# Kernel optimization log

Measured on AMD Instinct MI355X. Metric: run time of the kernel, lower is better.

## Reference

```python
import jax, jax.numpy as jnp
import numpy as np

B, T, D, H, NW = 2, 2048, 1024, 16, 64
HD = D // H  # 64
EPS = 1e-12  # F.normalize eps


def setup_inputs() -> dict:
    key = jax.random.key(0)
    ks = jax.random.split(key, 8)
    def lin(k, din, dout):
        return jax.random.normal(k, (din, dout), jnp.float32) / np.sqrt(din).astype(np.float32)
    return {
        "x": jax.random.normal(ks[0], (B, T, D), jnp.float32),
        "Wqf": lin(ks[1], D, H * NW), "bqf": jnp.zeros((H * NW,), jnp.float32),
        "Wkf": lin(ks[2], D, H * NW), "bkf": jnp.zeros((H * NW,), jnp.float32),
        "Wqp": lin(ks[3], D, H * NW), "bqp": jnp.zeros((H * NW,), jnp.float32),
        "Wkp": lin(ks[4], D, H * NW), "bkp": jnp.zeros((H * NW,), jnp.float32),
        "Wv": lin(ks[5], D, D), "bv": jnp.zeros((D,), jnp.float32),
        "Wo": lin(ks[6], D, D), "bo": jnp.zeros((D,), jnp.float32),
        "scale": jnp.ones((H, 1, 1), jnp.float32),  # interference_scale
    }


def reference(x, Wqf, bqf, Wkf, bkf, Wqp, bqp, Wkp, bkp, Wv, bv, Wo, bo, scale):
    Bx, Tx, Dx = x.shape
    def heads(W, b, nd):  # [B,T,H*nd] -> [B,H,T,nd]
        return jnp.transpose((x @ W + b).reshape(Bx, Tx, H, nd), (0, 2, 1, 3))
    qf = heads(Wqf, bqf, NW); kf = heads(Wkf, bkf, NW)
    qp = heads(Wqp, bqp, NW); kp = heads(Wkp, bkp, NW)
    v = heads(Wv, bv, HD)
    t = jnp.arange(Tx, dtype=x.dtype)[None, None, :, None]  # [1,1,T,1]
    def wave_norm(f, p):
        w = jnp.sin(f * t + p)  # [B,H,T,NW]
        n = jnp.sqrt(jnp.sum(w * w, axis=-1, keepdims=True))
        return w / jnp.maximum(n, EPS)
    qn = wave_norm(qf, qp)
    kn = wave_norm(kf, kp)
    inter = jnp.einsum('bhtw,bhsw->bhts', qn, kn) * scale[None]  # [B,H,T,T]
    causal = jnp.tril(jnp.ones((Tx, Tx), bool))  # keep diag and below
    inter = jnp.where(causal, inter, jnp.zeros((), x.dtype))
    denom = jnp.sqrt(jnp.arange(1, Tx + 1, dtype=x.dtype))[:, None]  # [T,1]
    attn = inter / denom
    # dropout is identity in eval mode
    out = jnp.einsum('bhts,bhsd->bhtd', attn, v)
    out = jnp.transpose(out, (0, 2, 1, 3)).reshape(Bx, Tx, Dx)
    return out @ Wo + bo
```

## Files before the change

kernel.cpp:

```cpp
#include <hip/hip_runtime.h>


#define Bb 2
#define Tt 2048
#define Dd 1024
#define Hh 16
#define NC 32

typedef _Float16 half_t;
typedef _Float16 half8 __attribute__((ext_vector_type(8)));
typedef _Float16 half4h __attribute__((ext_vector_type(4)));
typedef float f32x16 __attribute__((ext_vector_type(16)));

#define MFMA32(a, b, c) __builtin_amdgcn_mfma_f32_32x32x16_f16((a), (b), (c), 0, 0, 0)

#define GLL(G, L) __builtin_amdgcn_global_load_lds(                      \
    (const __attribute__((address_space(1))) void*)(G),                  \
    (__attribute__((address_space(3))) void*)(L), 16, 0, 0)

#define SCHED_FENCE() __builtin_amdgcn_sched_barrier(0)

#define BARC() {                                                         \
    asm volatile("s_waitcnt vmcnt(4) lgkmcnt(0)" ::: "memory");          \
    __builtin_amdgcn_s_barrier(); }

#define BAR_LG() {                                                       \
    SCHED_FENCE();                                                       \
    asm volatile("s_waitcnt lgkmcnt(0)" ::: "memory");                   \
    __builtin_amdgcn_s_barrier();                                        \
    SCHED_FENCE(); }

__global__ __launch_bounds__(256) void xsplit_kernel(
    const float* __restrict__ X, half_t* __restrict__ XHI, half_t* __restrict__ XLO)
{
  const size_t i = ((size_t)blockIdx.x * 256 + threadIdx.x) * 8;
  float4 a = *(const float4*)&X[i];
  float4 b = *(const float4*)&X[i + 4];
  const float av[8] = {a.x, a.y, a.z, a.w, b.x, b.y, b.z, b.w};
  half8 hv, lv;
  #pragma unroll
  for (int j = 0; j < 8; ++j) {
    half_t hx = (half_t)av[j];
    hv[j] = hx; lv[j] = (half_t)((av[j] - (float)hx) * 2048.f);
  }
  *(half8*)&XHI[i] = hv;
  *(half8*)&XLO[i] = lv;
}

__global__ __launch_bounds__(256) void wsplit_kernel(
    const float* __restrict__ W0, const float* __restrict__ W1,
    const float* __restrict__ W2, const float* __restrict__ W3,
    const float* __restrict__ W4, const float* __restrict__ W5,
    half_t* __restrict__ WSP)
{
  __shared__ float Ld[64][68];
  const int tid = threadIdx.x;
  const int m = blockIdx.z;
  const float* W = (m == 0) ? W0 : (m == 1) ? W1 : (m == 2) ? W2
                 : (m == 3) ? W3 : (m == 4) ? W4 : W5;
  const int k0 = blockIdx.x * 64, n0 = blockIdx.y * 64;
  const int r = tid >> 2, c4 = (tid & 3) * 16;
  #pragma unroll
  for (int i = 0; i < 4; ++i)
    *(float4*)&Ld[r][c4 + i * 4] =
        *(const float4*)&W[(size_t)(k0 + r) * Dd + n0 + c4 + i * 4];
  __syncthreads();
  half_t* hi = WSP + (size_t)m * 2097152;
  half_t* lo = hi + 1048576;
  const int n = tid >> 2, kc = (tid & 3) * 16;
  half8 hv0, hv1, lv0, lv1;
  #pragma unroll
  for (int i = 0; i < 8; ++i) {
    float v0 = Ld[kc + i][n];
    half_t h0 = (half_t)v0;
    hv0[i] = h0; lv0[i] = (half_t)((v0 - (float)h0) * 2048.f);
    float v1 = Ld[kc + 8 + i][n];
    half_t h1 = (half_t)v1;
    hv1[i] = h1; lv1[i] = (half_t)((v1 - (float)h1) * 2048.f);
  }
  *(half8*)&hi[(size_t)(n0 + n) * Dd + k0 + kc]     = hv0;
  *(half8*)&hi[(size_t)(n0 + n) * Dd + k0 + kc + 8] = hv1;
  *(half8*)&lo[(size_t)(n0 + n) * Dd + k0 + kc]     = lv0;
  *(half8*)&lo[(size_t)(n0 + n) * Dd + k0 + kc + 8] = lv1;
}

__global__ __launch_bounds__(256, 2) void proj_kernel(
    const half_t* __restrict__ XHI, const half_t* __restrict__ XLO,
    const half_t* __restrict__ WSP,
    const float* __restrict__ bqf, const float* __restrict__ bqp,
    const float* __restrict__ bkf, const float* __restrict__ bkp,
    half_t* __restrict__ QNH, half_t* __restrict__ KNH)
{
  __shared__ __align__(16) half_t Bs[4][128][64];
  const int tid = threadIdx.x;
  const int mb = blockIdx.x, h = blockIdx.y;
  const int b = blockIdx.z >> 1, p = blockIdx.z & 1;
  const int t0 = mb * 128, row0 = b * Tt + t0, col0 = h * 64;
  const half_t* WF = WSP + (size_t)(2 * p) * 2097152;
  const half_t* WP = WSP + (size_t)(2 * p + 1) * 2097152;
  const float* BF = p ? bkf : bqf;
  const float* BP = p ? bkp : bqp;
  half_t* OUTH = p ? KNH : QNH;

  f32x16 hh[4], mx[4];
  #pragma unroll
  for (int i = 0; i < 4; ++i) { hh[i] = (f32x16)(0.f); mx[i] = (f32x16)(0.f); }

  const int lane = tid & 63, w = tid >> 6;
  const int rl = lane & 31, kq = lane >> 5;
  const int sw = rl & 7;

  const half_t* aHi = XHI + (size_t)(row0 + 32 * w + rl) * Dd + kq * 8;
  const half_t* aLo = XLO + (size_t)(row0 + 32 * w + rl) * Dd + kq * 8;

  const int lr8 = lane >> 3;
  const int lcc = (lane & 7) ^ lr8;
  const int csel = (lcc & 3) * 8;
  const size_t loOff = (lcc >= 4) ? 1048576 : 0;
  const half_t* gb0 = WF + loOff + (size_t)(col0 + 8 * w + lr8) * Dd + csel;
  const half_t* gb1 = gb0 + 32 * Dd;
  const half_t* gb2 = WP + loOff + (size_t)(col0 + 8 * w + lr8) * Dd + csel;
  const half_t* gb3 = gb2 + 32 * Dd;

#define STAGE_PB(BI, K) {                          \
    GLL(gb0 + (K), &Bs[BI][8 * w][0]);             \
    GLL(gb1 + (K), &Bs[BI][32 + 8 * w][0]);        \
    GLL(gb2 + (K), &Bs[BI][64 + 8 * w][0]);        \
    GLL(gb3 + (K), &Bs[BI][96 + 8 * w][0]); }

#define LOADA(H0, H1, L0, L1, K) {                 \
    H0 = *(const half8*)&aHi[(K)];                 \
    H1 = *(const half8*)&aHi[(K) + 16];            \
    L0 = *(const half8*)&aLo[(K)];                 \
    L1 = *(const half8*)&aLo[(K) + 16]; }

#define KT_P(H0, H1, L0, L1, BI) {                                     \
    { const int c0 = (kq ^ sw) * 8, c1 = ((4 + kq) ^ sw) * 8;          \
      _Pragma("unroll")                                                \
      for (int tn = 0; tn < 4; ++tn) {                                 \
        half8 bh = *(const half8*)&Bs[BI][32 * tn + rl][c0];           \
        half8 bl = *(const half8*)&Bs[BI][32 * tn + rl][c1];           \
        hh[tn] = MFMA32(H0, bh, hh[tn]);                               \
        mx[tn] = MFMA32(H0, bl, mx[tn]);                               \
        mx[tn] = MFMA32(L0, bh, mx[tn]); } }                           \
    { const int c0 = (((2 + kq)) ^ sw) * 8, c1 = ((6 + kq) ^ sw) * 8;  \
      _Pragma("unroll")                                                \
      for (int tn = 0; tn < 4; ++tn) {                                 \
        half8 bh = *(const half8*)&Bs[BI][32 * tn + rl][c0];           \
        half8 bl = *(const half8*)&Bs[BI][32 * tn + rl][c1];           \
        hh[tn] = MFMA32(H1, bh, hh[tn]);                               \
        mx[tn] = MFMA32(H1, bl, mx[tn]);                               \
        mx[tn] = MFMA32(L1, bh, mx[tn]); } } }

  half8 ah0c, ah1c, al0c, al1c, ah0n, ah1n, al0n, al1n;
  STAGE_PB(0, 0)
  STAGE_PB(1, 32)
  LOADA(ah0c, ah1c, al0c, al1c, 0)
  BARC()

  #pragma unroll 1
  for (int k0 = 0; k0 < Dd; k0 += 128) {
    LOADA(ah0n, ah1n, al0n, al1n, k0 + 32)
    STAGE_PB(2, k0 + 64)
    KT_P(ah0c, ah1c, al0c, al1c, 0)
    BARC()
    LOADA(ah0c, ah1c, al0c, al1c, k0 + 64)
    STAGE_PB(3, k0 + 96)
    KT_P(ah0n, ah1n, al0n, al1n, 1)
    BARC()
    LOADA(ah0n, ah1n, al0n, al1n, k0 + 96)
    if (k0 + 128 < Dd) { STAGE_PB(0, k0 + 128) }
    KT_P(ah0c, ah1c, al0c, al1c, 2)
    BARC()
    if (k0 + 128 < Dd) { LOADA(ah0c, ah1c, al0c, al1c, k0 + 128) }
    if (k0 + 160 < Dd) { STAGE_PB(1, k0 + 160) }
    KT_P(ah0n, ah1n, al0n, al1n, 3)
    BARC()
  }
#undef STAGE_PB
#undef LOADA
#undef KT_P

  const float bf0 = BF[col0 + rl], bf1 = BF[col0 + 32 + rl];
  const float bp0 = BP[col0 + rl], bp1 = BP[col0 + 32 + rl];
  #pragma unroll
  for (int j = 0; j < 16; ++j) {
    const int rtj = (j & 3) + 8 * (j >> 2) + 4 * kq;
    const float tf = (float)(t0 + 32 * w + rtj);
    float f0 = hh[0][j] + mx[0][j] * (1.f / 2048.f) + bf0;
    float f1 = hh[1][j] + mx[1][j] * (1.f / 2048.f) + bf1;
    float p0 = hh[2][j] + mx[2][j] * (1.f / 2048.f) + bp0;
    float p1 = hh[3][j] + mx[3][j] * (1.f / 2048.f) + bp1;
    float w0 = sinf(fmaf(f0, tf, p0));
    float w1 = sinf(fmaf(f1, tf, p1));
    float ss = w0 * w0 + w1 * w1;
    ss += __shfl_xor(ss, 1); ss += __shfl_xor(ss, 2);
    ss += __shfl_xor(ss, 4); ss += __shfl_xor(ss, 8);
    ss += __shfl_xor(ss, 16);
    const float inv = 1.f / fmaxf(sqrtf(ss), 1e-12f);
    half_t* op = &OUTH[((size_t)(b * Tt) + t0 + 32 * w + rtj) * Dd + col0];
    op[rl]      = (half_t)(w0 * inv);
    op[32 + rl] = (half_t)(w1 * inv);
  }
}

__global__ __launch_bounds__(256, 2) void gemm_kernel(
    const half_t* __restrict__ AHI, const half_t* __restrict__ ALO,
    const half_t* __restrict__ WHI,
    const float* __restrict__ BIAS, float* __restrict__ OUT)
{
  __shared__ __align__(16) half_t As[2][128][64];
  __shared__ __align__(16) half_t Bs[2][128][64];
  const int tid = threadIdx.x;
  const int m0 = blockIdx.x * 128, n0 = blockIdx.y * 128;

  f32x16 hh[4], mx[4];
  #pragma unroll
  for (int i = 0; i < 4; ++i) { hh[i] = (f32x16)(0.f); mx[i] = (f32x16)(0.f); }

  const int lane = tid & 63, w = tid >> 6;
  const int rl = lane & 31, kq = lane >> 5;
  const int sw = rl & 7;

  const int r = tid & 127, isB = tid >> 7;
  const int swr = r & 7;
  const half_t* srcHi = isB ? &WHI[(size_t)(n0 + r) * Dd]
                            : &AHI[(size_t)(m0 + r) * Dd];
  const half_t* srcLo = isB ? &WHI[1048576 + (size_t)(n0 + r) * Dd]
                            : &ALO[(size_t)(m0 + r) * Dd];
  half_t* dstRow = isB ? &Bs[0][r][0] : &As[0][r][0];
  const int pc0 = (0 ^ swr) * 8, pc1 = (1 ^ swr) * 8;
  const int pc2 = (2 ^ swr) * 8, pc3 = (3 ^ swr) * 8;
  const int pc4 = (4 ^ swr) * 8, pc5 = (5 ^ swr) * 8;
  const int pc6 = (6 ^ swr) * 8, pc7 = (7 ^ swr) * 8;

  half8 rg0, rg1, rg2, rg3, rg4, rg5, rg6, rg7;

#define G_LOADREGS(K)                                                          \
  rg0 = *(const half8*)&srcHi[(K)];      rg1 = *(const half8*)&srcHi[(K) + 8]; \
  rg2 = *(const half8*)&srcHi[(K) + 16]; rg3 = *(const half8*)&srcHi[(K) + 24];\
  rg4 = *(const half8*)&srcLo[(K)];      rg5 = *(const half8*)&srcLo[(K) + 8]; \
  rg6 = *(const half8*)&srcLo[(K) + 16]; rg7 = *(const half8*)&srcLo[(K) + 24];

#define G_WRITE(BI) {                                                     \
  half_t* d_ = dstRow + (BI) * 8192;                                      \
  *(half8*)&d_[pc0] = rg0; *(half8*)&d_[pc1] = rg1;                       \
  *(half8*)&d_[pc2] = rg2; *(half8*)&d_[pc3] = rg3;                       \
  *(half8*)&d_[pc4] = rg4; *(half8*)&d_[pc5] = rg5;                       \
  *(half8*)&d_[pc6] = rg6; *(half8*)&d_[pc7] = rg7; }

#define G_KT(BI)                                                          \
  _Pragma("unroll")                                                       \
  for (int ks = 0; ks < 2; ++ks) {                                        \
    half8 ahi = *(const half8*)&As[BI][32 * w + rl][((2 * ks + kq) ^ sw) * 8];       \
    half8 alo = *(const half8*)&As[BI][32 * w + rl][((4 + 2 * ks + kq) ^ sw) * 8];   \
    _Pragma("unroll")                                                     \
    for (int tn = 0; tn < 4; ++tn) {                                      \
      half8 bhi = *(const half8*)&Bs[BI][32 * tn + rl][((2 * ks + kq) ^ sw) * 8];    \
      half8 blo = *(const half8*)&Bs[BI][32 * tn + rl][((4 + 2 * ks + kq) ^ sw) * 8];\
      hh[tn] = MFMA32(ahi, bhi, hh[tn]);                                  \
      mx[tn] = MFMA32(ahi, blo, mx[tn]);                                  \
      mx[tn] = MFMA32(alo, bhi, mx[tn]);                                  \
    }                                                                     \
  }

  G_LOADREGS(0)
  G_WRITE(0)
  G_LOADREGS(32)
  BAR_LG()

  #pragma unroll 1
  for (int k0 = 0; k0 < Dd; k0 += 64) {
    G_KT(0)
    G_WRITE(1)
    if (k0 + 64 < Dd) { G_LOADREGS(k0 + 64) }
    BAR_LG()
    G_KT(1)
    if (k0 + 64 < Dd) { G_WRITE(0) }
    if (k0 + 96 < Dd) { G_LOADREGS(k0 + 96) }
    BAR_LG()
  }
#undef G_LOADREGS
#undef G_WRITE
#undef G_KT

  const float bb0 = BIAS[n0 + rl],      bb1 = BIAS[n0 + 32 + rl];
  const float bb2 = BIAS[n0 + 64 + rl], bb3 = BIAS[n0 + 96 + rl];
  #pragma unroll
  for (int j = 0; j < 16; ++j) {
    const int rtj = (j & 3) + 8 * (j >> 2) + 4 * kq;
    float* orow = &OUT[(size_t)(m0 + 32 * w + rtj) * Dd + n0];
    orow[rl]      = hh[0][j] + mx[0][j] * (1.f / 2048.f) + bb0;
    orow[32 + rl] = hh[1][j] + mx[1][j] * (1.f / 2048.f) + bb1;
    orow[64 + rl] = hh[2][j] + mx[2][j] * (1.f / 2048.f) + bb2;
    orow[96 + rl] = hh[3][j] + mx[3][j] * (1.f / 2048.f) + bb3;
  }
}

__global__ __launch_bounds__(256) void chunk_kv_kernel(
    const half_t* __restrict__ KNH, const float* __restrict__ V,
    float* __restrict__ G)
{
  __shared__ float Ks[64][64];
  __shared__ float Vs[64][64];
  const int tid = threadIdx.x;
  const int c = blockIdx.x, h = blockIdx.y, b = blockIdx.z;
  const int s0 = c * 64;
  const int lr = tid >> 2, lc = (tid & 3) * 16;
  {
    const half_t* krow = &KNH[(size_t)(b * Tt + s0 + lr) * Dd + h * 64 + lc];
    half8 ka = *(const half8*)&krow[0];
    half8 kb = *(const half8*)&krow[8];
    #pragma unroll
    for (int i = 0; i < 8; ++i) {
      Ks[lr][lc + i] = (float)ka[i];
      Ks[lr][lc + 8 + i] = (float)kb[i];
    }
    const float* vrow = &V[(size_t)(b * Tt + s0 + lr) * Dd + h * 64 + lc];
    #pragma unroll
    for (int i = 0; i < 4; ++i)
      *(float4*)&Vs[lr][lc + i * 4] = *(const float4*)&vrow[i * 4];
  }
  __syncthreads();

  const int ty = tid >> 4, tx = tid & 15;
  float g[4][4] = {{0.f}};
  #pragma unroll 4
  for (int s = 0; s < 64; ++s) {
    float4 kv = *(const float4*)&Ks[s][ty * 4];
    float4 vv = *(const float4*)&Vs[s][tx * 4];
    const float* k_ = (const float*)&kv;
    const float* v_ = (const float*)&vv;
    #pragma unroll
    for (int i = 0; i < 4; ++i)
      #pragma unroll
      for (int j = 0; j < 4; ++j)
        g[i][j] = fmaf(k_[i], v_[j], g[i][j]);
  }
  float* Gp = G + (((size_t)(b * Hh + h) * NC + c) << 12);
  #pragma unroll
  for (int i = 0; i < 4; ++i)
    *(float4*)&Gp[(ty * 4 + i) * 64 + tx * 4] =
        make_float4(g[i][0], g[i][1], g[i][2], g[i][3]);
}

__global__ __launch_bounds__(256) void prefix_kernel(float* __restrict__ G)
{
  const int seg = blockIdx.x, h = blockIdx.y, b = blockIdx.z;
  float* base = G + (((size_t)(b * Hh + h) * NC) << 12) + seg * 256 + threadIdx.x;
  float acc = 0.f;
  #pragma unroll 4
  for (int c = 0; c < NC; ++c) {
    float* p = base + ((size_t)c << 12);
    const float g = *p;
    *p = acc;
    acc += g;
  }
}

__global__ __launch_bounds__(256) void attn_chunk_kernel(
    const half_t* __restrict__ QNH, const half_t* __restrict__ KNH,
    const float* __restrict__ V, const float* __restrict__ M,
    const float* __restrict__ SCALE,
    half_t* __restrict__ ATTHI, half_t* __restrict__ ATTLO)
{
  __shared__ float Qt[64][68];
  __shared__ float Kt[64][68];
  __shared__ float SM[64][68];
  __shared__ float Vs[64][64];
  const int tid = threadIdx.x;
  const int c = blockIdx.x, h = blockIdx.y, b = blockIdx.z;
  const int t0 = c * 64;
  const int lr = tid >> 2, lc = (tid & 3) * 16;
  {
    const half_t* qrow = &QNH[(size_t)(b * Tt + t0 + lr) * Dd + h * 64 + lc];
    const half_t* krow = &KNH[(size_t)(b * Tt + t0 + lr) * Dd + h * 64 + lc];
    half8 qa = *(const half8*)&qrow[0];
    half8 qb = *(const half8*)&qrow[8];
    half8 ka = *(const half8*)&krow[0];
    half8 kb = *(const half8*)&krow[8];
    #pragma unroll
    for (int i = 0; i < 8; ++i) {
      Qt[lc + i][lr] = (float)qa[i];     Qt[lc + 8 + i][lr] = (float)qb[i];
      Kt[lc + i][lr] = (float)ka[i];     Kt[lc + 8 + i][lr] = (float)kb[i];
    }
    const float* vrow = &V[(size_t)(b * Tt + t0 + lr) * Dd + h * 64 + lc];
    const float* mrow = &M[(((size_t)(b * Hh + h) * NC + c) << 12) + lr * 64 + lc];
    #pragma unroll
    for (int i = 0; i < 4; ++i) {
      *(float4*)&Vs[lr][lc + i * 4] = *(const float4*)&vrow[i * 4];
      *(float4*)&SM[lr][lc + i * 4] = *(const float4*)&mrow[i * 4];
    }
  }
  __syncthreads();

  const int ty = tid >> 4, tx = tid & 15;
  float o[4][4] = {{0.f}};
  float sc[4][4] = {{0.f}};

  #pragma unroll 4
  for (int w = 0; w < 64; ++w) {
    float4 qv = *(const float4*)&Qt[w][ty * 4];
    float4 mv = *(const float4*)&SM[w][tx * 4];
    float4 kv = *(const float4*)&Kt[w][tx * 4];
    const float* q_ = (const float*)&qv;
    const float* m_ = (const float*)&mv;
    const float* k_ = (const float*)&kv;
    #pragma unroll
    for (int i = 0; i < 4; ++i) {
      float qq = q_[i];
      #pragma unroll
      for (int j = 0; j < 4; ++j) {
        o[i][j]  = fmaf(qq, m_[j], o[i][j]);
        sc[i][j] = fmaf(qq, k_[j], sc[i][j]);
      }
    }
  }
  __syncthreads();

  #pragma unroll
  for (int i = 0; i < 4; ++i) {
    const int lt = ty * 4 + i;
    #pragma unroll
    for (int j = 0; j < 4; ++j) {
      const int ls = tx * 4 + j;
      SM[ls][lt] = (ls <= lt) ? sc[i][j] : 0.f;
    }
  }
  __syncthreads();

  #pragma unroll 4
  for (int s = 0; s < 64; ++s) {
    float4 sv = *(const float4*)&SM[s][ty * 4];
    float4 vv = *(const float4*)&Vs[s][tx * 4];
    const float* s_ = (const float*)&sv;
    const float* v_ = (const float*)&vv;
    #pragma unroll
    for (int i = 0; i < 4; ++i)
      #pragma unroll
      for (int j = 0; j < 4; ++j)
        o[i][j] = fmaf(s_[i], v_[j], o[i][j]);
  }

  const float sch = SCALE[h];
  #pragma unroll
  for (int i = 0; i < 4; ++i) {
    const int t = t0 + ty * 4 + i;
    const float fac = sch / sqrtf((float)(t + 1));
    half4h hv, lv;
    #pragma unroll
    for (int j = 0; j < 4; ++j) {
      float v = o[i][j] * fac;
      half_t hx = (half_t)v;
      hv[j] = hx; lv[j] = (half_t)((v - (float)hx) * 2048.f);
    }
    *(half4h*)&ATTHI[(size_t)(b * Tt + t) * Dd + h * 64 + tx * 4] = hv;
    *(half4h*)&ATTLO[(size_t)(b * Tt + t) * Dd + h * 64 + tx * 4] = lv;
  }
}

extern "C" void kernel_launch(void* const* d_in, const int* in_sizes, int n_in,
                              void* d_out, int out_size, void* d_ws, size_t ws_size,
                              hipStream_t stream) {
  const float* x   = (const float*)d_in[0];
  const float* Wqf = (const float*)d_in[1];
  const float* bqf = (const float*)d_in[2];
  const float* Wkf = (const float*)d_in[3];
  const float* bkf = (const float*)d_in[4];
  const float* Wqp = (const float*)d_in[5];
  const float* bqp = (const float*)d_in[6];
  const float* Wkp = (const float*)d_in[7];
  const float* bkp = (const float*)d_in[8];
  const float* Wv  = (const float*)d_in[9];
  const float* bv  = (const float*)d_in[10];
  const float* Wo  = (const float*)d_in[11];
  const float* bo  = (const float*)d_in[12];
  const float* scale = (const float*)d_in[13];

  half_t* WSP = (half_t*)d_ws;
  half_t* qnh = WSP + 12582912;
  half_t* knh = qnh + 4194304;
  float*  G   = (float*)(knh + 4194304);
  half_t* xhi = (half_t*)G;
  half_t* xlo = xhi + 4194304;
  float*  vbuf = (float*)d_out;

  xsplit_kernel<<<dim3(2048), 256, 0, stream>>>(x, xhi, xlo);

  wsplit_kernel<<<dim3(16, 16, 6), 256, 0, stream>>>(Wqf, Wqp, Wkf, Wkp, Wv, Wo, WSP);

  proj_kernel<<<dim3(Tt / 128, Hh, Bb * 2), 256, 0, stream>>>(
      xhi, xlo, WSP, bqf, bqp, bkf, bkp, qnh, knh);

  gemm_kernel<<<dim3((Bb * Tt) / 128, Dd / 128), 256, 0, stream>>>(
      xhi, xlo, WSP + (size_t)4 * 2097152, bv, vbuf);

  chunk_kv_kernel<<<dim3(NC, Hh, Bb), 256, 0, stream>>>(knh, vbuf, G);
  prefix_kernel<<<dim3(16, Hh, Bb), 256, 0, stream>>>(G);
  attn_chunk_kernel<<<dim3(NC, Hh, Bb), 256, 0, stream>>>(
      qnh, knh, vbuf, G, scale, qnh , knh );

  gemm_kernel<<<dim3((Bb * Tt) / 128, Dd / 128), 256, 0, stream>>>(
      qnh, knh, WSP + (size_t)5 * 2097152, bo, (float*)d_out);
}
```

Baseline: 360.5 us.

## Double proj kernel M-tile to 256 rows per block to reuse staged weights

Each wave in the projection kernel now computes two 32-row sub-tiles (64 rows) instead of one, so a block covers 256 time steps and each staged weight tile in shared memory feeds twice as many MFMAs. The grid along T is halved and launch bounds drop to one block per SM to make room for the doubled accumulators. This cuts weight re-fetch from global memory and LDS traffic per FLOP. In exchange it raises register pressure, halves the block count to 512, and loses the latency hiding that two resident blocks provided.

```diff
diff --git a/kernel.cpp b/kernel.cpp
--- a/kernel.cpp
+++ b/kernel.cpp
@@ -84,7 +84,7 @@
   *(half8*)&lo[(size_t)(n0 + n) * Dd + k0 + kc + 8] = lv1;
 }
 
-__global__ __launch_bounds__(256, 2) void proj_kernel(
+__global__ __launch_bounds__(256, 1) void proj_kernel(
     const half_t* __restrict__ XHI, const half_t* __restrict__ XLO,
     const half_t* __restrict__ WSP,
     const float* __restrict__ bqf, const float* __restrict__ bqp,
@@ -95,23 +95,28 @@
   const int tid = threadIdx.x;
   const int mb = blockIdx.x, h = blockIdx.y;
   const int b = blockIdx.z >> 1, p = blockIdx.z & 1;
-  const int t0 = mb * 128, row0 = b * Tt + t0, col0 = h * 64;
+  const int t0 = mb * 256, row0 = b * Tt + t0, col0 = h * 64;
   const half_t* WF = WSP + (size_t)(2 * p) * 2097152;
   const half_t* WP = WSP + (size_t)(2 * p + 1) * 2097152;
   const float* BF = p ? bkf : bqf;
   const float* BP = p ? bkp : bqp;
   half_t* OUTH = p ? KNH : QNH;
 
-  f32x16 hh[4], mx[4];
-  #pragma unroll
-  for (int i = 0; i < 4; ++i) { hh[i] = (f32x16)(0.f); mx[i] = (f32x16)(0.f); }
+  f32x16 hh0[4], mx0[4], hh1[4], mx1[4];
+  #pragma unroll
+  for (int i = 0; i < 4; ++i) {
+    hh0[i] = (f32x16)(0.f); mx0[i] = (f32x16)(0.f);
+    hh1[i] = (f32x16)(0.f); mx1[i] = (f32x16)(0.f);
+  }
 
   const int lane = tid & 63, w = tid >> 6;
   const int rl = lane & 31, kq = lane >> 5;
   const int sw = rl & 7;
 
-  const half_t* aHi = XHI + (size_t)(row0 + 32 * w + rl) * Dd + kq * 8;
-  const half_t* aLo = XLO + (size_t)(row0 + 32 * w + rl) * Dd + kq * 8;
+  const half_t* aHi0 = XHI + (size_t)(row0 + 64 * w + rl) * Dd + kq * 8;
+  const half_t* aLo0 = XLO + (size_t)(row0 + 64 * w + rl) * Dd + kq * 8;
+  const half_t* aHi1 = aHi0 + 32 * Dd;
+  const half_t* aLo1 = aLo0 + 32 * Dd;
 
   const int lr8 = lane >> 3;
   const int lcc = (lane & 7) ^ lr8;
@@ -128,79 +133,94 @@
     GLL(gb2 + (K), &Bs[BI][64 + 8 * w][0]);        \
     GLL(gb3 + (K), &Bs[BI][96 + 8 * w][0]); }
 
-#define LOADA(H0, H1, L0, L1, K) {                 \
-    H0 = *(const half8*)&aHi[(K)];                 \
-    H1 = *(const half8*)&aHi[(K) + 16];            \
-    L0 = *(const half8*)&aLo[(K)];                 \
-    L1 = *(const half8*)&aLo[(K) + 16]; }
-
-#define KT_P(H0, H1, L0, L1, BI) {                                     \
+#define LOADA8(R00, R01, R02, R03, R10, R11, R12, R13, K) {  \
+    R00 = *(const half8*)&aHi0[(K)];                         \
+    R01 = *(const half8*)&aHi0[(K) + 16];                    \
+    R02 = *(const half8*)&aLo0[(K)];                         \
+    R03 = *(const half8*)&aLo0[(K) + 16];                    \
+    R10 = *(const half8*)&aHi1[(K)];                         \
+    R11 = *(const half8*)&aHi1[(K) + 16];                    \
+    R12 = *(const half8*)&aLo1[(K)];                         \
+    R13 = *(const half8*)&aLo1[(K) + 16]; }
+
+#define KT2(R00, R01, R02, R03, R10, R11, R12, R13, BI) {              \
     { const int c0 = (kq ^ sw) * 8, c1 = ((4 + kq) ^ sw) * 8;          \
       _Pragma("unroll")                                                \
       for (int tn = 0; tn < 4; ++tn) {                                 \
         half8 bh = *(const half8*)&Bs[BI][32 * tn + rl][c0];           \
         half8 bl = *(const half8*)&Bs[BI][32 * tn + rl][c1];           \
-        hh[tn] = MFMA32(H0, bh, hh[tn]);                               \
-        mx[tn] = MFMA32(H0, bl, mx[tn]);                               \
-        mx[tn] = MFMA32(L0, bh, mx[tn]); } }                           \
-    { const int c0 = (((2 + kq)) ^ sw) * 8, c1 = ((6 + kq) ^ sw) * 8;  \
+        hh0[tn] = MFMA32(R00, bh, hh0[tn]);                            \
+        mx0[tn] = MFMA32(R00, bl, mx0[tn]);                            \
+        mx0[tn] = MFMA32(R02, bh, mx0[tn]);                            \
+        hh1[tn] = MFMA32(R10, bh, hh1[tn]);                            \
+        mx1[tn] = MFMA32(R10, bl, mx1[tn]);                            \
+        mx1[tn] = MFMA32(R12, bh, mx1[tn]); } }                        \
+    { const int c0 = ((2 + kq) ^ sw) * 8, c1 = ((6 + kq) ^ sw) * 8;    \
       _Pragma("unroll")                                                \
       for (int tn = 0; tn < 4; ++tn) {                                 \
         half8 bh = *(const half8*)&Bs[BI][32 * tn + rl][c0];           \
         half8 bl = *(const half8*)&Bs[BI][32 * tn + rl][c1];           \
-        hh[tn] = MFMA32(H1, bh, hh[tn]);                               \
-        mx[tn] = MFMA32(H1, bl, mx[tn]);                               \
-        mx[tn] = MFMA32(L1, bh, mx[tn]); } } }
-
-  half8 ah0c, ah1c, al0c, al1c, ah0n, ah1n, al0n, al1n;
+        hh0[tn] = MFMA32(R01, bh, hh0[tn]);                            \
+        mx0[tn] = MFMA32(R01, bl, mx0[tn]);                            \
+        mx0[tn] = MFMA32(R03, bh, mx0[tn]);                            \
+        hh1[tn] = MFMA32(R11, bh, hh1[tn]);                            \
+        mx1[tn] = MFMA32(R11, bl, mx1[tn]);                            \
+        mx1[tn] = MFMA32(R13, bh, mx1[tn]); } } }
+
+  half8 c00, c01, c02, c03, c10, c11, c12, c13;
+  half8 n00, n01, n02, n03, n10, n11, n12, n13;
   STAGE_PB(0, 0)
   STAGE_PB(1, 32)
-  LOADA(ah0c, ah1c, al0c, al1c, 0)
+  LOADA8(c00, c01, c02, c03, c10, c11, c12, c13, 0)
   BARC()
 
   #pragma unroll 1
   for (int k0 = 0; k0 < Dd; k0 += 128) {
-    LOADA(ah0n, ah1n, al0n, al1n, k0 + 32)
+    LOADA8(n00, n01, n02, n03, n10, n11, n12, n13, k0 + 32)
     STAGE_PB(2, k0 + 64)
-    KT_P(ah0c, ah1c, al0c, al1c, 0)
+    KT2(c00, c01, c02, c03, c10, c11, c12, c13, 0)
     BARC()
-    LOADA(ah0c, ah1c, al0c, al1c, k0 + 64)
+    LOADA8(c00, c01, c02, c03, c10, c11, c12, c13, k0 + 64)
     STAGE_PB(3, k0 + 96)
-    KT_P(ah0n, ah1n, al0n, al1n, 1)
+    KT2(n00, n01, n02, n03, n10, n11, n12, n13, 1)
     BARC()
-    LOADA(ah0n, ah1n, al0n, al1n, k0 + 96)
+    LOADA8(n00, n01, n02, n03, n10, n11, n12, n13, k0 + 96)
     if (k0 + 128 < Dd) { STAGE_PB(0, k0 + 128) }
-    KT_P(ah0c, ah1c, al0c, al1c, 2)
+    KT2(c00, c01, c02, c03, c10, c11, c12, c13, 2)
     BARC()
-    if (k0 + 128 < Dd) { LOADA(ah0c, ah1c, al0c, al1c, k0 + 128) }
+    if (k0 + 128 < Dd) { LOADA8(c00, c01, c02, c03, c10, c11, c12, c13, k0 + 128) }
     if (k0 + 160 < Dd) { STAGE_PB(1, k0 + 160) }
-    KT_P(ah0n, ah1n, al0n, al1n, 3)
+    KT2(n00, n01, n02, n03, n10, n11, n12, n13, 3)
     BARC()
   }
 #undef STAGE_PB
-#undef LOADA
-#undef KT_P
+#undef LOADA8
+#undef KT2
 
   const float bf0 = BF[col0 + rl], bf1 = BF[col0 + 32 + rl];
   const float bp0 = BP[col0 + rl], bp1 = BP[col0 + 32 + rl];
   #pragma unroll
-  for (int j = 0; j < 16; ++j) {
-    const int rtj = (j & 3) + 8 * (j >> 2) + 4 * kq;
-    const float tf = (float)(t0 + 32 * w + rtj);
-    float f0 = hh[0][j] + mx[0][j] * (1.f / 2048.f) + bf0;
-    float f1 = hh[1][j] + mx[1][j] * (1.f / 2048.f) + bf1;
-    float p0 = hh[2][j] + mx[2][j] * (1.f / 2048.f) + bp0;
-    float p1 = hh[3][j] + mx[3][j] * (1.f / 2048.f) + bp1;
-    float w0 = sinf(fmaf(f0, tf, p0));
-    float w1 = sinf(fmaf(f1, tf, p1));
-    float ss = w0 * w0 + w1 * w1;
-    ss += __shfl_xor(ss, 1); ss += __shfl_xor(ss, 2);
-    ss += __shfl_xor(ss, 4); ss += __shfl_xor(ss, 8);
-    ss += __shfl_xor(ss, 16);
-    const float inv = 1.f / fmaxf(sqrtf(ss), 1e-12f);
-    half_t* op = &OUTH[((size_t)(b * Tt) + t0 + 32 * w + rtj) * Dd + col0];
-    op[rl]      = (half_t)(w0 * inv);
-    op[32 + rl] = (half_t)(w1 * inv);
+  for (int g = 0; g < 2; ++g) {
+    #pragma unroll
+    for (int j = 0; j < 16; ++j) {
+      const int rtj = (j & 3) + 8 * (j >> 2) + 4 * kq;
+      const int trow = t0 + 64 * w + 32 * g + rtj;
+      const float tf = (float)trow;
+      float f0 = (g ? hh1[0][j] : hh0[0][j]) + (g ? mx1[0][j] : mx0[0][j]) * (1.f / 2048.f) + bf0;
+      float f1 = (g ? hh1[1][j] : hh0[1][j]) + (g ? mx1[1][j] : mx0[1][j]) * (1.f / 2048.f) + bf1;
+      float p0 = (g ? hh1[2][j] : hh0[2][j]) + (g ? mx1[2][j] : mx0[2][j]) * (1.f / 2048.f) + bp0;
+      float p1 = (g ? hh1[3][j] : hh0[3][j]) + (g ? mx1[3][j] : mx0[3][j]) * (1.f / 2048.f) + bp1;
+      float w0 = sinf(fmaf(f0, tf, p0));
+      float w1 = sinf(fmaf(f1, tf, p1));
+      float ss = w0 * w0 + w1 * w1;
+      ss += __shfl_xor(ss, 1); ss += __shfl_xor(ss, 2);
+      ss += __shfl_xor(ss, 4); ss += __shfl_xor(ss, 8);
+      ss += __shfl_xor(ss, 16);
+      const float inv = 1.f / fmaxf(sqrtf(ss), 1e-12f);
+      half_t* op = &OUTH[((size_t)(b * Tt) + trow) * Dd + col0];
+      op[rl]      = (half_t)(w0 * inv);
+      op[32 + rl] = (half_t)(w1 * inv);
+    }
   }
 }
 
@@ -489,7 +509,7 @@
 
   wsplit_kernel<<<dim3(16, 16, 6), 256, 0, stream>>>(Wqf, Wqp, Wkf, Wkp, Wv, Wo, WSP);
 
-  proj_kernel<<<dim3(Tt / 128, Hh, Bb * 2), 256, 0, stream>>>(
+  proj_kernel<<<dim3(Tt / 256, Hh, Bb * 2), 256, 0, stream>>>(
       xhi, xlo, WSP, bqf, bqp, bkf, bkp, qnh, knh);
 
   gemm_kernel<<<dim3((Bb * Tt) / 128, Dd / 128), 256, 0, stream>>>(
```

Measured after the change: 423.7 us. +17.5%, slower.

## Merge split kernels and merge QK projection with V GEMM into single launches

Applied to the files above, without the earlier changes.

Combines the x-split and weight-split kernels into one launch with block-index dispatch. It also merges the Q/K wave projection kernel and the V projection GEMM into a single kernel whose blocks branch on their index and share one LDS buffer. This cuts launch count and lets the two projection workloads run concurrently to fill the GPU better. The cost is that both branches now share the higher LDS and register footprint, which may reduce occupancy for one of them.

```diff
diff --git a/kernel.cpp b/kernel.cpp
--- a/kernel.cpp
+++ b/kernel.cpp
@@ -30,35 +30,37 @@
     __builtin_amdgcn_s_barrier();                                        \
     SCHED_FENCE(); }
 
-__global__ __launch_bounds__(256) void xsplit_kernel(
-    const float* __restrict__ X, half_t* __restrict__ XHI, half_t* __restrict__ XLO)
-{
-  const size_t i = ((size_t)blockIdx.x * 256 + threadIdx.x) * 8;
-  float4 a = *(const float4*)&X[i];
-  float4 b = *(const float4*)&X[i + 4];
-  const float av[8] = {a.x, a.y, a.z, a.w, b.x, b.y, b.z, b.w};
-  half8 hv, lv;
-  #pragma unroll
-  for (int j = 0; j < 8; ++j) {
-    half_t hx = (half_t)av[j];
-    hv[j] = hx; lv[j] = (half_t)((av[j] - (float)hx) * 2048.f);
-  }
-  *(half8*)&XHI[i] = hv;
-  *(half8*)&XLO[i] = lv;
-}
-
-__global__ __launch_bounds__(256) void wsplit_kernel(
+__global__ __launch_bounds__(256) void xwsplit_kernel(
+    const float* __restrict__ X,
     const float* __restrict__ W0, const float* __restrict__ W1,
     const float* __restrict__ W2, const float* __restrict__ W3,
     const float* __restrict__ W4, const float* __restrict__ W5,
+    half_t* __restrict__ XHI, half_t* __restrict__ XLO,
     half_t* __restrict__ WSP)
 {
   __shared__ float Ld[64][68];
   const int tid = threadIdx.x;
-  const int m = blockIdx.z;
+  const int bid = blockIdx.x;
+  if (bid < 2048) {
+    const size_t i = ((size_t)bid * 256 + tid) * 8;
+    float4 a = *(const float4*)&X[i];
+    float4 b = *(const float4*)&X[i + 4];
+    const float av[8] = {a.x, a.y, a.z, a.w, b.x, b.y, b.z, b.w};
+    half8 hv, lv;
+    #pragma unroll
+    for (int j = 0; j < 8; ++j) {
+      half_t hx = (half_t)av[j];
+      hv[j] = hx; lv[j] = (half_t)((av[j] - (float)hx) * 2048.f);
+    }
+    *(half8*)&XHI[i] = hv;
+    *(half8*)&XLO[i] = lv;
+    return;
+  }
+  const int idx = bid - 2048;
+  const int m = idx >> 8;
   const float* W = (m == 0) ? W0 : (m == 1) ? W1 : (m == 2) ? W2
                  : (m == 3) ? W3 : (m == 4) ? W4 : W5;
-  const int k0 = blockIdx.x * 64, n0 = blockIdx.y * 64;
+  const int k0 = (idx & 15) * 64, n0 = ((idx >> 4) & 15) * 64;
   const int r = tid >> 2, c4 = (tid & 3) * 16;
   #pragma unroll
   for (int i = 0; i < 4; ++i)
@@ -84,43 +86,48 @@
   *(half8*)&lo[(size_t)(n0 + n) * Dd + k0 + kc + 8] = lv1;
 }
 
-__global__ __launch_bounds__(256, 2) void proj_kernel(
+__global__ __launch_bounds__(256, 2) void projv_kernel(
     const half_t* __restrict__ XHI, const half_t* __restrict__ XLO,
     const half_t* __restrict__ WSP,
     const float* __restrict__ bqf, const float* __restrict__ bqp,
     const float* __restrict__ bkf, const float* __restrict__ bkp,
-    half_t* __restrict__ QNH, half_t* __restrict__ KNH)
+    half_t* __restrict__ QNH, half_t* __restrict__ KNH,
+    const float* __restrict__ BV, float* __restrict__ VOUT)
 {
-  __shared__ __align__(16) half_t Bs[4][128][64];
+  __shared__ __align__(16) half_t LDSU[32768];
   const int tid = threadIdx.x;
-  const int mb = blockIdx.x, h = blockIdx.y;
-  const int b = blockIdx.z >> 1, p = blockIdx.z & 1;
-  const int t0 = mb * 128, row0 = b * Tt + t0, col0 = h * 64;
-  const half_t* WF = WSP + (size_t)(2 * p) * 2097152;
-  const half_t* WP = WSP + (size_t)(2 * p + 1) * 2097152;
-  const float* BF = p ? bkf : bqf;
-  const float* BP = p ? bkp : bqp;
-  half_t* OUTH = p ? KNH : QNH;
-
-  f32x16 hh[4], mx[4];
-  #pragma unroll
-  for (int i = 0; i < 4; ++i) { hh[i] = (f32x16)(0.f); mx[i] = (f32x16)(0.f); }
-
+  const int bid = blockIdx.x;
   const int lane = tid & 63, w = tid >> 6;
   const int rl = lane & 31, kq = lane >> 5;
   const int sw = rl & 7;
 
-  const half_t* aHi = XHI + (size_t)(row0 + 32 * w + rl) * Dd + kq * 8;
-  const half_t* aLo = XLO + (size_t)(row0 + 32 * w + rl) * Dd + kq * 8;
-
-  const int lr8 = lane >> 3;
-  const int lcc = (lane & 7) ^ lr8;
-  const int csel = (lcc & 3) * 8;
-  const size_t loOff = (lcc >= 4) ? 1048576 : 0;
-  const half_t* gb0 = WF + loOff + (size_t)(col0 + 8 * w + lr8) * Dd + csel;
-  const half_t* gb1 = gb0 + 32 * Dd;
-  const half_t* gb2 = WP + loOff + (size_t)(col0 + 8 * w + lr8) * Dd + csel;
-  const half_t* gb3 = gb2 + 32 * Dd;
+  if (bid < 1024) {
+    half_t (*Bs)[128][64] = (half_t (*)[128][64])LDSU;
+    const int mb = bid & 15, h = (bid >> 4) & 15;
+    const int z = bid >> 8;
+    const int b = z >> 1, p = z & 1;
+    const int t0 = mb * 128, row0 = b * Tt + t0, col0 = h * 64;
+    const half_t* WF = WSP + (size_t)(2 * p) * 2097152;
+    const half_t* WP = WSP + (size_t)(2 * p + 1) * 2097152;
+    const float* BF = p ? bkf : bqf;
+    const float* BP = p ? bkp : bqp;
+    half_t* OUTH = p ? KNH : QNH;
+
+    f32x16 hh[4], mx[4];
+    #pragma unroll
+    for (int i = 0; i < 4; ++i) { hh[i] = (f32x16)(0.f); mx[i] = (f32x16)(0.f); }
+
+    const half_t* aHi = XHI + (size_t)(row0 + 32 * w + rl) * Dd + kq * 8;
+    const half_t* aLo = XLO + (size_t)(row0 + 32 * w + rl) * Dd + kq * 8;
+
+    const int lr8 = lane >> 3;
+    const int lcc = (lane & 7) ^ lr8;
+    const int csel = (lcc & 3) * 8;
+    const size_t loOff = (lcc >= 4) ? 1048576 : 0;
+    const half_t* gb0 = WF + loOff + (size_t)(col0 + 8 * w + lr8) * Dd + csel;
+    const half_t* gb1 = gb0 + 32 * Dd;
+    const half_t* gb2 = WP + loOff + (size_t)(col0 + 8 * w + lr8) * Dd + csel;
+    const half_t* gb3 = gb2 + 32 * Dd;
 
 #define STAGE_PB(BI, K) {                          \
     GLL(gb0 + (K), &Bs[BI][8 * w][0]);             \
@@ -152,55 +159,143 @@
         mx[tn] = MFMA32(H1, bl, mx[tn]);                               \
         mx[tn] = MFMA32(L1, bh, mx[tn]); } } }
 
-  half8 ah0c, ah1c, al0c, al1c, ah0n, ah1n, al0n, al1n;
-  STAGE_PB(0, 0)
-  STAGE_PB(1, 32)
-  LOADA(ah0c, ah1c, al0c, al1c, 0)
-  BARC()
-
-  #pragma unroll 1
-  for (int k0 = 0; k0 < Dd; k0 += 128) {
-    LOADA(ah0n, ah1n, al0n, al1n, k0 + 32)
-    STAGE_PB(2, k0 + 64)
-    KT_P(ah0c, ah1c, al0c, al1c, 0)
+    half8 ah0c, ah1c, al0c, al1c, ah0n, ah1n, al0n, al1n;
+    STAGE_PB(0, 0)
+    STAGE_PB(1, 32)
+    LOADA(ah0c, ah1c, al0c, al1c, 0)
     BARC()
-    LOADA(ah0c, ah1c, al0c, al1c, k0 + 64)
-    STAGE_PB(3, k0 + 96)
-    KT_P(ah0n, ah1n, al0n, al1n, 1)
-    BARC()
-    LOADA(ah0n, ah1n, al0n, al1n, k0 + 96)
-    if (k0 + 128 < Dd) { STAGE_PB(0, k0 + 128) }
-    KT_P(ah0c, ah1c, al0c, al1c, 2)
-    BARC()
-    if (k0 + 128 < Dd) { LOADA(ah0c, ah1c, al0c, al1c, k0 + 128) }
-    if (k0 + 160 < Dd) { STAGE_PB(1, k0 + 160) }
-    KT_P(ah0n, ah1n, al0n, al1n, 3)
-    BARC()
-  }
+
+    #pragma unroll 1
+    for (int k0 = 0; k0 < Dd; k0 += 128) {
+      LOADA(ah0n, ah1n, al0n, al1n, k0 + 32)
+      STAGE_PB(2, k0 + 64)
+      KT_P(ah0c, ah1c, al0c, al1c, 0)
+      BARC()
+      LOADA(ah0c, ah1c, al0c, al1c, k0 + 64)
+      STAGE_PB(3, k0 + 96)
+      KT_P(ah0n, ah1n, al0n, al1n, 1)
+      BARC()
+      LOADA(ah0n, ah1n, al0n, al1n, k0 + 96)
+      if (k0 + 128 < Dd) { STAGE_PB(0, k0 + 128) }
+      KT_P(ah0c, ah1c, al0c, al1c, 2)
+      BARC()
+      if (k0 + 128 < Dd) { LOADA(ah0c, ah1c, al0c, al1c, k0 + 128) }
+      if (k0 + 160 < Dd) { STAGE_PB(1, k0 + 160) }
+      KT_P(ah0n, ah1n, al0n, al1n, 3)
+      BARC()
+    }
 #undef STAGE_PB
 #undef LOADA
 #undef KT_P
 
-  const float bf0 = BF[col0 + rl], bf1 = BF[col0 + 32 + rl];
-  const float bp0 = BP[col0 + rl], bp1 = BP[col0 + 32 + rl];
-  #pragma unroll
-  for (int j = 0; j < 16; ++j) {
-    const int rtj = (j & 3) + 8 * (j >> 2) + 4 * kq;
-    const float tf = (float)(t0 + 32 * w + rtj);
-    float f0 = hh[0][j] + mx[0][j] * (1.f / 2048.f) + bf0;
-    float f1 = hh[1][j] + mx[1][j] * (1.f / 2048.f) + bf1;
-    float p0 = hh[2][j] + mx[2][j] * (1.f / 2048.f) + bp0;
-    float p1 = hh[3][j] + mx[3][j] * (1.f / 2048.f) + bp1;
-    float w0 = sinf(fmaf(f0, tf, p0));
-    float w1 = sinf(fmaf(f1, tf, p1));
-    float ss = w0 * w0 + w1 * w1;
-    ss += __shfl_xor(ss, 1); ss += __shfl_xor(ss, 2);
-    ss += __shfl_xor(ss, 4); ss += __shfl_xor(ss, 8);
-    ss += __shfl_xor(ss, 16);
-    const float inv = 1.f / fmaxf(sqrtf(ss), 1e-12f);
-    half_t* op = &OUTH[((size_t)(b * Tt) + t0 + 32 * w + rtj) * Dd + col0];
-    op[rl]      = (half_t)(w0 * inv);
-    op[32 + rl] = (half_t)(w1 * inv);
+    const float bf0 = BF[col0 + rl], bf1 = BF[col0 + 32 + rl];
+    const float bp0 = BP[col0 + rl], bp1 = BP[col0 + 32 + rl];
+    #pragma unroll
+    for (int j = 0; j < 16; ++j) {
+      const int rtj = (j & 3) + 8 * (j >> 2) + 4 * kq;
+      const float tf = (float)(t0 + 32 * w + rtj);
+      float f0 = hh[0][j] + mx[0][j] * (1.f / 2048.f) + bf0;
+      float f1 = hh[1][j] + mx[1][j] * (1.f / 2048.f) + bf1;
+      float p0 = hh[2][j] + mx[2][j] * (1.f / 2048.f) + bp0;
+      float p1 = hh[3][j] + mx[3][j] * (1.f / 2048.f) + bp1;
+      float w0 = sinf(fmaf(f0, tf, p0));
+      float w1 = sinf(fmaf(f1, tf, p1));
+      float ss = w0 * w0 + w1 * w1;
+      ss += __shfl_xor(ss, 1); ss += __shfl_xor(ss, 2);
+      ss += __shfl_xor(ss, 4); ss += __shfl_xor(ss, 8);
+      ss += __shfl_xor(ss, 16);
+      const float inv = 1.f / fmaxf(sqrtf(ss), 1e-12f);
+      half_t* op = &OUTH[((size_t)(b * Tt) + t0 + 32 * w + rtj) * Dd + col0];
+      op[rl]      = (half_t)(w0 * inv);
+      op[32 + rl] = (half_t)(w1 * inv);
+    }
+    return;
+  }
+
+  {
+    half_t (*AsG)[128][64] = (half_t (*)[128][64])LDSU;
+    half_t (*BsG)[128][64] = (half_t (*)[128][64])(LDSU + 16384);
+    const half_t* WHI = WSP + (size_t)4 * 2097152;
+    const int g = bid - 1024;
+    const int m0 = (g & 31) * 128, n0 = (g >> 5) * 128;
+
+    f32x16 hh[4], mx[4];
+    #pragma unroll
+    for (int i = 0; i < 4; ++i) { hh[i] = (f32x16)(0.f); mx[i] = (f32x16)(0.f); }
+
+    const int r = tid & 127, isB = tid >> 7;
+    const int swr = r & 7;
+    const half_t* srcHi = isB ? &WHI[(size_t)(n0 + r) * Dd]
+                              : &XHI[(size_t)(m0 + r) * Dd];
+    const half_t* srcLo = isB ? &WHI[1048576 + (size_t)(n0 + r) * Dd]
+                              : &XLO[(size_t)(m0 + r) * Dd];
+    half_t* dstRow = isB ? &BsG[0][r][0] : &AsG[0][r][0];
+    const int pc0 = (0 ^ swr) * 8, pc1 = (1 ^ swr) * 8;
+    const int pc2 = (2 ^ swr) * 8, pc3 = (3 ^ swr) * 8;
+    const int pc4 = (4 ^ swr) * 8, pc5 = (5 ^ swr) * 8;
+    const int pc6 = (6 ^ swr) * 8, pc7 = (7 ^ swr) * 8;
+
+    half8 rg0, rg1, rg2, rg3, rg4, rg5, rg6, rg7;
+
+#define G_LOADREGS(K)                                                          \
+  rg0 = *(const half8*)&srcHi[(K)];      rg1 = *(const half8*)&srcHi[(K) + 8]; \
+  rg2 = *(const half8*)&srcHi[(K) + 16]; rg3 = *(const half8*)&srcHi[(K) + 24];\
+  rg4 = *(const half8*)&srcLo[(K)];      rg5 = *(const half8*)&srcLo[(K) + 8]; \
+  rg6 = *(const half8*)&srcLo[(K) + 16]; rg7 = *(const half8*)&srcLo[(K) + 24];
+
+#define G_WRITE(BI) {                                                     \
+  half_t* d_ = dstRow + (BI) * 8192;                                      \
+  *(half8*)&d_[pc0] = rg0; *(half8*)&d_[pc1] = rg1;                       \
+  *(half8*)&d_[pc2] = rg2; *(half8*)&d_[pc3] = rg3;                       \
+  *(half8*)&d_[pc4] = rg4; *(half8*)&d_[pc5] = rg5;                       \
+  *(half8*)&d_[pc6] = rg6; *(half8*)&d_[pc7] = rg7; }
+
+#define G_KT(BI)                                                          \
+  _Pragma("unroll")                                                       \
+  for (int ks = 0; ks < 2; ++ks) {                                        \
+    half8 ahi = *(const half8*)&AsG[BI][32 * w + rl][((2 * ks + kq) ^ sw) * 8];       \
+    half8 alo = *(const half8*)&AsG[BI][32 * w + rl][((4 + 2 * ks + kq) ^ sw) * 8];   \
+    _Pragma("unroll")                                                     \
+    for (int tn = 0; tn < 4; ++tn) {                                      \
+      half8 bhi = *(const half8*)&BsG[BI][32 * tn + rl][((2 * ks + kq) ^ sw) * 8];    \
+      half8 blo = *(const half8*)&BsG[BI][32 * tn + rl][((4 + 2 * ks + kq) ^ sw) * 8];\
+      hh[tn] = MFMA32(ahi, bhi, hh[tn]);                                  \
+      mx[tn] = MFMA32(ahi, blo, mx[tn]);                                  \
+      mx[tn] = MFMA32(alo, bhi, mx[tn]);                                  \
+    }                                                                     \
+  }
+
+    G_LOADREGS(0)
+    G_WRITE(0)
+    G_LOADREGS(32)
+    BAR_LG()
+
+    #pragma unroll 1
+    for (int k0 = 0; k0 < Dd; k0 += 64) {
+      G_KT(0)
+      G_WRITE(1)
+      if (k0 + 64 < Dd) { G_LOADREGS(k0 + 64) }
+      BAR_LG()
+      G_KT(1)
+      if (k0 + 64 < Dd) { G_WRITE(0) }
+      if (k0 + 96 < Dd) { G_LOADREGS(k0 + 96) }
+      BAR_LG()
+    }
+#undef G_LOADREGS
+#undef G_WRITE
+#undef G_KT
+
+    const float bb0 = BV[n0 + rl],      bb1 = BV[n0 + 32 + rl];
+    const float bb2 = BV[n0 + 64 + rl], bb3 = BV[n0 + 96 + rl];
+    #pragma unroll
+    for (int j = 0; j < 16; ++j) {
+      const int rtj = (j & 3) + 8 * (j >> 2) + 4 * kq;
+      float* orow = &VOUT[(size_t)(m0 + 32 * w + rtj) * Dd + n0];
+      orow[rl]      = hh[0][j] + mx[0][j] * (1.f / 2048.f) + bb0;
+      orow[32 + rl] = hh[1][j] + mx[1][j] * (1.f / 2048.f) + bb1;
+      orow[64 + rl] = hh[2][j] + mx[2][j] * (1.f / 2048.f) + bb2;
+      orow[96 + rl] = hh[3][j] + mx[3][j] * (1.f / 2048.f) + bb3;
+    }
   }
 }
 
@@ -485,15 +580,11 @@
   half_t* xlo = xhi + 4194304;
   float*  vbuf = (float*)d_out;
 
-  xsplit_kernel<<<dim3(2048), 256, 0, stream>>>(x, xhi, xlo);
-
-  wsplit_kernel<<<dim3(16, 16, 6), 256, 0, stream>>>(Wqf, Wqp, Wkf, Wkp, Wv, Wo, WSP);
-
-  proj_kernel<<<dim3(Tt / 128, Hh, Bb * 2), 256, 0, stream>>>(
-      xhi, xlo, WSP, bqf, bqp, bkf, bkp, qnh, knh);
-
-  gemm_kernel<<<dim3((Bb * Tt) / 128, Dd / 128), 256, 0, stream>>>(
-      xhi, xlo, WSP + (size_t)4 * 2097152, bv, vbuf);
+  xwsplit_kernel<<<dim3(2048 + 1536), 256, 0, stream>>>(
+      x, Wqf, Wqp, Wkf, Wkp, Wv, Wo, xhi, xlo, WSP);
+
+  projv_kernel<<<dim3(1024 + 256), 256, 0, stream>>>(
+      xhi, xlo, WSP, bqf, bqp, bkf, bkp, qnh, knh, bv, vbuf);
 
   chunk_kv_kernel<<<dim3(NC, Hh, Bb), 256, 0, stream>>>(knh, vbuf, G);
   prefix_kernel<<<dim3(16, Hh, Bb), 256, 0, stream>>>(G);
```

Measured after the change: 345.1 us. 1.04x faster.
